# Optimization experiments

Hardware: AMD Instinct MI355X
Metric: run time of the kernel (lower is better)

Reference implementation:

```python
import jax, jax.numpy as jnp
import numpy as np

KSIZE = 3
STRIDE = 1
PADDING = 1
DILATION = 1
C_IN = 16
C_OUT = 16


def setup_inputs() -> dict:
    key = jax.random.key(0)
    k1, k2, k3 = jax.random.split(key, 3)
    inputs = jax.random.normal(k1, (2, C_IN, 24, 24, 24, 24), dtype=jnp.float32)
    weight = jax.random.normal(k2, (C_OUT, C_IN * KSIZE ** 4), dtype=jnp.float32)
    bias = jax.random.normal(k3, (1, C_OUT, 1, 1, 1, 1), dtype=jnp.float32)
    return {"inputs": inputs, "weight": weight, "bias": bias}


def reference(inputs, weight, bias):
    # weight stored flattened: [C_out, C_in * k^4] -> [C_out, C_in, k, k, k, k]
    w = weight.reshape(C_OUT, C_IN, KSIZE, KSIZE, KSIZE, KSIZE)
    # General 4-spatial-dim convolution via XLA's ND conv.
    dn = jax.lax.ConvDimensionNumbers(
        lhs_spec=(0, 1, 2, 3, 4, 5),   # N, C, U, V, H, W
        rhs_spec=(0, 1, 2, 3, 4, 5),   # O, I, kU, kV, kH, kW
        out_spec=(0, 1, 2, 3, 4, 5),
    )
    out = jax.lax.conv_general_dilated(
        inputs, w,
        window_strides=(STRIDE,) * 4,
        padding=((PADDING, PADDING),) * 4,
        rhs_dilation=(DILATION,) * 4,
        dimension_numbers=dn,
    )
    return out + bias
```

## Files before the change

kernel.cpp:

```cpp
#include <hip/hip_runtime.h>

#define S 24
#define PLANE 576
#define CISTRIDE 331776
#define SLAB_B 21632
#define QSLAB_B 6656
#define QOFF 4992
#define A_BYTES 46080
#define WS_SLABS A_BYTES

typedef __attribute__((ext_vector_type(8))) short bf16x8;
typedef __attribute__((ext_vector_type(4))) float f32x4;

__device__ __forceinline__ ushort f2bf(float f) {
    unsigned int u = __builtin_bit_cast(unsigned int, f);
    unsigned int r = u + 0x7fffu + ((u >> 16) & 1u);
    return (ushort)(r >> 16);
}

__device__ __forceinline__ int swz(int row, int col, int half) {
    return (((row * 26 + col) * 32) + half * 16) ^ ((row & 3) << 4);
}

__global__ void __launch_bounds__(256)
pack_in(const float* __restrict__ in, const float* __restrict__ wgt, char* __restrict__ ws) {
    __shared__ unsigned lds_t[16][288];

    const int b = blockIdx.x;
    const int nb = b / PLANE, uv = b % PLANE;
    const float* src = in + (size_t)nb * 16 * CISTRIDE + (size_t)uv * PLANE;
    char* dst = ws + WS_SLABS + (size_t)b * SLAB_B;
    const int t = threadIdx.x;

    float4 f[9];
    #pragma unroll
    for (int i = 0; i < 9; ++i) {
        int flat = i * 256 + t;
        int ci = flat / 144, q4 = flat % 144;
        f[i] = *(const float4*)(src + (size_t)ci * CISTRIDE + 4 * q4);
    }
    #pragma unroll
    for (int i = 0; i < 9; ++i) {
        int flat = i * 256 + t;
        int ci = flat / 144, q4 = flat % 144;
        uint2 pk;
        pk.x = (unsigned)f2bf(f[i].x) | ((unsigned)f2bf(f[i].y) << 16);
        pk.y = (unsigned)f2bf(f[i].z) | ((unsigned)f2bf(f[i].w) << 16);
        *(uint2*)&lds_t[ci][2 * q4] = pk;
    }
    __syncthreads();

    #pragma unroll
    for (int i = 0; i < 6; ++i) {
        int c = i * 256 + t;
        if (c < 1352) {
            int k = c >> 2;
            int row = k / 13;
            int pos2 = c ^ (row & 3);
            int pos = pos2 >> 1, h = pos2 & 1;
            int col = pos - row * 26;
            uint4 o = make_uint4(0, 0, 0, 0);
            if (row >= 1 && row <= 24 && col >= 1 && col <= 24) {
                int q = (row - 1) * 24 + (col - 1);
                int q2 = q >> 1, odd = q & 1;
                #pragma unroll
                for (int kk = 0; kk < 4; ++kk) {
                    unsigned a = lds_t[8 * h + 2 * kk][q2];
                    unsigned bb = lds_t[8 * h + 2 * kk + 1][q2];
                    unsigned val = odd ? ((a >> 16) | (bb & 0xffff0000u))
                                       : ((a & 0xffffu) | (bb << 16));
                    ((unsigned*)&o)[kk] = val;
                }
            }
            *(uint4*)(dst + (size_t)c * 16) = o;
        }
    }

    if (b == 0) {
        for (int i = t; i < 2880; i += 256) {
            int step = i >> 6;
            int tap = step / 5, s = step % 5;
            int lane = i & 63;
            int co = lane & 15, gA = lane >> 4;
            int o = 2 * s + (gA >> 1);
            int cib = (gA & 1) * 8;
            ushort vals[8];
            #pragma unroll
            for (int j = 0; j < 8; ++j)
                vals[j] = (o <= 8) ? f2bf(wgt[co * 1296 + (cib + j) * 81 + tap * 9 + o]) : (ushort)0;
            uint4 pk;
            pk.x = vals[0] | ((unsigned)vals[1] << 16);
            pk.y = vals[2] | ((unsigned)vals[3] << 16);
            pk.z = vals[4] | ((unsigned)vals[5] << 16);
            pk.w = vals[6] | ((unsigned)vals[7] << 16);
            *(uint4*)(ws + (size_t)i * 16) = pk;
        }
    }
}

__global__ void __launch_bounds__(192, 4)
conv4d_main(const char* __restrict__ ws, const float* __restrict__ bias,
            float* __restrict__ out) {
    __shared__ __align__(16) char lds[2 * QSLAB_B];

    const int t = threadIdx.x, lane = t & 63, wvid = t >> 6;
    const int braw = blockIdx.x;
    const int b = (braw & 7) * 288 + (braw >> 3);
    const int nb = b / 1152, rem = b % 1152;
    const int u = rem / 48, rem2 = rem % 48;
    const int v0 = (rem2 >> 2) * 2, qq = rem2 & 3;

    const int n16 = lane & 15, g = lane >> 4;
    const int dh = n16 >> 3, dw = n16 & 7;
    const int half = g & 1, osel = g >> 1;

    int laneoff[2][5];
    #pragma unroll
    for (int trp = 0; trp < 2; ++trp)
        #pragma unroll
        for (int s = 0; s < 5; ++s) {
            int o = 2 * s + osel; if (o > 8) o = 8;
            int kh = o / 3, kw = o % 3;
            int r_off = dh + kh, c_off = dw + kw;
            int lin = (r_off * 26 + c_off) * 32 + half * 16;
            laneoff[trp][s] = lin ^ ((((trp << 1) + r_off) & 3) << 4);
        }

    f32x4 acc0[3], acc1[3];
    #pragma unroll
    for (int i = 0; i < 3; ++i) { acc0[i] = (f32x4){0,0,0,0}; acc1[i] = (f32x4){0,0,0,0}; }

    unsigned mask = 0;
    #pragma unroll
    for (int i = 0; i < 12; ++i) {
        int uu = u + (i >> 2) - 1, vv = v0 + (i & 3) - 1;
        if (uu >= 0 && uu < S && vv >= 0 && vv < S) mask |= 1u << i;
    }

    const char* slabs = ws + WS_SLABS;
    const int srcoff = qq * QOFF;
    #define SLAB_PTR(i_) (slabs + ((size_t)nb * PLANE + (u + ((i_) >> 2) - 1) * S + (v0 + ((i_) & 3) - 1)) * SLAB_B + srcoff)

    #define STAGE(bufsel_, src_) do {                                              \
        const char* _s = (src_);                                                   \
        _Pragma("unroll")                                                          \
        for (int r2 = 0; r2 < 3; ++r2) {                                           \
            int chunk = r2 * 192 + t;                                              \
            if (r2 < 2 || t < 32)                                                  \
                __builtin_amdgcn_global_load_lds(                                  \
                    (const __attribute__((address_space(1))) unsigned int*)(_s + (size_t)chunk * 16), \
                    (__attribute__((address_space(3))) unsigned int*)(lds + (bufsel_) * QSLAB_B + chunk * 16), \
                    16, 0, 0);                                                     \
        }                                                                          \
    } while (0)

    const bf16x8 zfr = {0,0,0,0,0,0,0,0};

    int cur = __ffs(mask) - 1;
    int bufsel = 0;
    STAGE(0, SLAB_PTR(cur));
    __syncthreads();

    while (1) {
        unsigned remm = mask >> (cur + 1);
        int nxt = remm ? (cur + 1 + __ffs(remm) - 1) : -1;

        const int ku = cur >> 2, dv = (cur & 3) - 1;
        const bool v0ok = dv <= 1, v1ok = dv >= 0;
        const int t0i = min(ku * 3 + dv + 1, 8);
        const int t1i = max(ku * 3 + dv, 0);
        const char* ap0 = ws + (size_t)t0i * 5120 + (size_t)lane * 16;
        const char* ap1 = ws + (size_t)t1i * 5120 + (size_t)lane * 16;
        bf16x8 afr0[5], afr1[5];
        #pragma unroll
        for (int s = 0; s < 5; ++s) {
            bf16x8 r0 = *(const bf16x8*)(ap0 + s * 1024);
            bf16x8 r1 = *(const bf16x8*)(ap1 + s * 1024);
            afr0[s] = v0ok ? r0 : zfr;
            afr1[s] = v1ok ? r1 : zfr;
        }
        __builtin_amdgcn_sched_barrier(0);

        if (nxt >= 0) STAGE(bufsel ^ 1, SLAB_PTR(nxt));

        const char* bp = lds + bufsel * QSLAB_B + wvid * 256;
        #pragma unroll
        for (int tr = 0; tr < 3; ++tr) {
            const int trp = (tr + qq) & 1;
            const char* bpt = bp + tr * 1664;
            #pragma unroll
            for (int s = 0; s < 5; ++s) {
                bf16x8 bfr = *(const bf16x8*)(bpt + laneoff[trp][s]);
                acc0[tr] = __builtin_amdgcn_mfma_f32_16x16x32_bf16(afr0[s], bfr, acc0[tr], 0, 0, 0);
                acc1[tr] = __builtin_amdgcn_mfma_f32_16x16x32_bf16(afr1[s], bfr, acc1[tr], 0, 0, 0);
            }
        }
        __syncthreads();
        if (nxt < 0) break;
        cur = nxt; bufsel ^= 1;
    }

    float bv[4];
    #pragma unroll
    for (int r = 0; r < 4; ++r) bv[r] = bias[g * 4 + r];
    float* outp0 = out + (size_t)nb * 16 * CISTRIDE + (size_t)(u * S + v0) * PLANE;
    float* outp1 = outp0 + PLANE;
    #pragma unroll
    for (int tr = 0; tr < 3; ++tr) {
        int row = qq * 6 + tr * 2 + dh;
        int col = wvid * 8 + dw;
        int pos = row * S + col;
        #pragma unroll
        for (int r = 0; r < 4; ++r) {
            outp0[(size_t)(g * 4 + r) * CISTRIDE + pos] = acc0[tr][r] + bv[r];
            outp1[(size_t)(g * 4 + r) * CISTRIDE + pos] = acc1[tr][r] + bv[r];
        }
    }
}

extern "C" void kernel_launch(void* const* d_in, const int* in_sizes, int n_in,
                              void* d_out, int out_size, void* d_ws, size_t ws_size,
                              hipStream_t stream) {
    const float* in   = (const float*)d_in[0];
    const float* wgt  = (const float*)d_in[1];
    const float* bias = (const float*)d_in[2];
    float* out        = (float*)d_out;
    char* ws          = (char*)d_ws;

    pack_in<<<dim3(1152), dim3(256), 0, stream>>>(in, wgt, ws);
    conv4d_main<<<dim3(2304), dim3(192), 0, stream>>>(ws, bias, out);
}
```

Before: 82.87 us.

## Deepen conv slab pipeline to two-ahead prefetch and use a zero weight slab

The main loop now prefetches the LDS input slab two taps ahead into the buffer just consumed. It loads the next tap's weight fragments before a single barrier per iteration, using an explicit vmcnt wait in place of a full __syncthreads. Out-of-range taps point at an extra all-zero weight slab written by the pack kernel, which removes the per-fragment selects. The aim is to hide global-load latency behind the MFMA work and cut synchronisation. In exchange it relies on hand-counted vmcnt values being correct and holds more registers live.

```diff
diff --git a/kernel.cpp b/kernel.cpp
--- a/kernel.cpp
+++ b/kernel.cpp
@@ -6,7 +6,7 @@
 #define SLAB_B 21632
 #define QSLAB_B 6656
 #define QOFF 4992
-#define A_BYTES 46080
+#define A_BYTES 51200
 #define WS_SLABS A_BYTES
 
 typedef __attribute__((ext_vector_type(8))) short bf16x8;
@@ -16,10 +16,6 @@
     unsigned int u = __builtin_bit_cast(unsigned int, f);
     unsigned int r = u + 0x7fffu + ((u >> 16) & 1u);
     return (ushort)(r >> 16);
-}
-
-__device__ __forceinline__ int swz(int row, int col, int half) {
-    return (((row * 26 + col) * 32) + half * 16) ^ ((row & 3) << 4);
 }
 
 __global__ void __launch_bounds__(256)
@@ -77,7 +73,7 @@
     }
 
     if (b == 0) {
-        for (int i = t; i < 2880; i += 256) {
+        for (int i = t; i < 3200; i += 256) {
             int step = i >> 6;
             int tap = step / 5, s = step % 5;
             int lane = i & 63;
@@ -86,8 +82,11 @@
             int cib = (gA & 1) * 8;
             ushort vals[8];
             #pragma unroll
-            for (int j = 0; j < 8; ++j)
-                vals[j] = (o <= 8) ? f2bf(wgt[co * 1296 + (cib + j) * 81 + tap * 9 + o]) : (ushort)0;
+            for (int j = 0; j < 8; ++j) {
+                int widx = co * 1296 + (cib + j) * 81 + tap * 9 + o;
+                widx = widx < 20736 ? widx : 0;
+                vals[j] = (tap <= 8 && o <= 8) ? f2bf(wgt[widx]) : (ushort)0;
+            }
             uint4 pk;
             pk.x = vals[0] | ((unsigned)vals[1] << 16);
             pk.y = vals[2] | ((unsigned)vals[3] << 16);
@@ -154,36 +153,33 @@
         }                                                                          \
     } while (0)
 
-    const bf16x8 zfr = {0,0,0,0,0,0,0,0};
+    bf16x8 a0[5], a1[5];
+    #define LOAD_A(tap_) do {                                                      \
+        int _ku = (tap_) >> 2, _dv = ((tap_) & 3) - 1;                             \
+        int _s0 = (_dv <= 1) ? (_ku * 3 + _dv + 1) : 9;                            \
+        int _s1 = (_dv >= 0) ? (_ku * 3 + _dv) : 9;                                \
+        const char* _ap0 = ws + (size_t)_s0 * 5120 + (size_t)lane * 16;            \
+        const char* _ap1 = ws + (size_t)_s1 * 5120 + (size_t)lane * 16;            \
+        _Pragma("unroll")                                                          \
+        for (int s = 0; s < 5; ++s) {                                              \
+            a0[s] = *(const bf16x8*)(_ap0 + s * 1024);                             \
+            a1[s] = *(const bf16x8*)(_ap1 + s * 1024);                             \
+        }                                                                          \
+    } while (0)
 
     int cur = __ffs(mask) - 1;
-    int bufsel = 0;
+    unsigned remm = mask >> (cur + 1);
+    int nxt = remm ? (cur + 1 + __ffs(remm) - 1) : -1;
+
     STAGE(0, SLAB_PTR(cur));
-    __syncthreads();
-
+    LOAD_A(cur);
+    if (nxt >= 0) STAGE(1, SLAB_PTR(nxt));
+    asm volatile("s_waitcnt vmcnt(10)" ::: "memory");
+    __builtin_amdgcn_s_barrier();
+
+    int cb = 0;
     while (1) {
-        unsigned remm = mask >> (cur + 1);
-        int nxt = remm ? (cur + 1 + __ffs(remm) - 1) : -1;
-
-        const int ku = cur >> 2, dv = (cur & 3) - 1;
-        const bool v0ok = dv <= 1, v1ok = dv >= 0;
-        const int t0i = min(ku * 3 + dv + 1, 8);
-        const int t1i = max(ku * 3 + dv, 0);
-        const char* ap0 = ws + (size_t)t0i * 5120 + (size_t)lane * 16;
-        const char* ap1 = ws + (size_t)t1i * 5120 + (size_t)lane * 16;
-        bf16x8 afr0[5], afr1[5];
-        #pragma unroll
-        for (int s = 0; s < 5; ++s) {
-            bf16x8 r0 = *(const bf16x8*)(ap0 + s * 1024);
-            bf16x8 r1 = *(const bf16x8*)(ap1 + s * 1024);
-            afr0[s] = v0ok ? r0 : zfr;
-            afr1[s] = v1ok ? r1 : zfr;
-        }
-        __builtin_amdgcn_sched_barrier(0);
-
-        if (nxt >= 0) STAGE(bufsel ^ 1, SLAB_PTR(nxt));
-
-        const char* bp = lds + bufsel * QSLAB_B + wvid * 256;
+        const char* bp = lds + cb * QSLAB_B + wvid * 256;
         #pragma unroll
         for (int tr = 0; tr < 3; ++tr) {
             const int trp = (tr + qq) & 1;
@@ -191,13 +187,18 @@
             #pragma unroll
             for (int s = 0; s < 5; ++s) {
                 bf16x8 bfr = *(const bf16x8*)(bpt + laneoff[trp][s]);
-                acc0[tr] = __builtin_amdgcn_mfma_f32_16x16x32_bf16(afr0[s], bfr, acc0[tr], 0, 0, 0);
-                acc1[tr] = __builtin_amdgcn_mfma_f32_16x16x32_bf16(afr1[s], bfr, acc1[tr], 0, 0, 0);
+                acc0[tr] = __builtin_amdgcn_mfma_f32_16x16x32_bf16(a0[s], bfr, acc0[tr], 0, 0, 0);
+                acc1[tr] = __builtin_amdgcn_mfma_f32_16x16x32_bf16(a1[s], bfr, acc1[tr], 0, 0, 0);
             }
         }
-        __syncthreads();
         if (nxt < 0) break;
-        cur = nxt; bufsel ^= 1;
+        unsigned r2m = mask >> (nxt + 1);
+        int nxt2 = r2m ? (nxt + 1 + __ffs(r2m) - 1) : -1;
+        LOAD_A(nxt);
+        asm volatile("s_waitcnt vmcnt(10)" ::: "memory");
+        __builtin_amdgcn_s_barrier();
+        if (nxt2 >= 0) STAGE(cb, SLAB_PTR(nxt2));
+        cur = nxt; nxt = nxt2; cb ^= 1;
     }
 
     float bv[4];
```

Result: faster. 80.78 us (-2.5%).

## Compute four output v-planes per block to reuse staged input slabs

Applied to the files above, without the earlier changes.

The main conv kernel now has each block produce four adjacent v output planes instead of two. It walks 18 input slabs per ku, holds all three kv weight fragments in registers, and accumulates into 12 tiles, halving the grid and cutting redundant slab staging per output. The pack kernel now loads fp32 straight into LDS with global_load_lds and converts to bf16 when writing the swizzled output. The trade-off is higher register pressure, reflected in the occupancy hint dropping from 4 to 3, and fewer blocks in flight.

```diff
diff --git a/kernel.cpp b/kernel.cpp
--- a/kernel.cpp
+++ b/kernel.cpp
@@ -18,13 +18,9 @@
     return (ushort)(r >> 16);
 }
 
-__device__ __forceinline__ int swz(int row, int col, int half) {
-    return (((row * 26 + col) * 32) + half * 16) ^ ((row & 3) << 4);
-}
-
 __global__ void __launch_bounds__(256)
 pack_in(const float* __restrict__ in, const float* __restrict__ wgt, char* __restrict__ ws) {
-    __shared__ unsigned lds_t[16][288];
+    __shared__ __align__(16) float lds_f[16 * 576];
 
     const int b = blockIdx.x;
     const int nb = b / PLANE, uv = b % PLANE;
@@ -32,21 +28,14 @@
     char* dst = ws + WS_SLABS + (size_t)b * SLAB_B;
     const int t = threadIdx.x;
 
-    float4 f[9];
-    #pragma unroll
-    for (int i = 0; i < 9; ++i) {
-        int flat = i * 256 + t;
-        int ci = flat / 144, q4 = flat % 144;
-        f[i] = *(const float4*)(src + (size_t)ci * CISTRIDE + 4 * q4);
-    }
-    #pragma unroll
-    for (int i = 0; i < 9; ++i) {
-        int flat = i * 256 + t;
-        int ci = flat / 144, q4 = flat % 144;
-        uint2 pk;
-        pk.x = (unsigned)f2bf(f[i].x) | ((unsigned)f2bf(f[i].y) << 16);
-        pk.y = (unsigned)f2bf(f[i].z) | ((unsigned)f2bf(f[i].w) << 16);
-        *(uint2*)&lds_t[ci][2 * q4] = pk;
+    #pragma unroll
+    for (int r = 0; r < 9; ++r) {
+        int chunk = r * 256 + t;
+        int ci = chunk / 144, q4 = chunk % 144;
+        __builtin_amdgcn_global_load_lds(
+            (const __attribute__((address_space(1))) unsigned int*)(src + (size_t)ci * CISTRIDE + 4 * q4),
+            (__attribute__((address_space(3))) unsigned int*)(&lds_f[chunk * 4]),
+            16, 0, 0);
     }
     __syncthreads();
 
@@ -54,25 +43,19 @@
     for (int i = 0; i < 6; ++i) {
         int c = i * 256 + t;
         if (c < 1352) {
-            int k = c >> 2;
-            int row = k / 13;
-            int pos2 = c ^ (row & 3);
-            int pos = pos2 >> 1, h = pos2 & 1;
-            int col = pos - row * 26;
+            int pos = c >> 1, h = c & 1;
+            int row = pos / 26, col = pos % 26;
             uint4 o = make_uint4(0, 0, 0, 0);
             if (row >= 1 && row <= 24 && col >= 1 && col <= 24) {
                 int q = (row - 1) * 24 + (col - 1);
-                int q2 = q >> 1, odd = q & 1;
                 #pragma unroll
                 for (int kk = 0; kk < 4; ++kk) {
-                    unsigned a = lds_t[8 * h + 2 * kk][q2];
-                    unsigned bb = lds_t[8 * h + 2 * kk + 1][q2];
-                    unsigned val = odd ? ((a >> 16) | (bb & 0xffff0000u))
-                                       : ((a & 0xffffu) | (bb << 16));
-                    ((unsigned*)&o)[kk] = val;
+                    float fa = lds_f[(8 * h + 2 * kk) * 576 + q];
+                    float fb = lds_f[(8 * h + 2 * kk + 1) * 576 + q];
+                    ((unsigned*)&o)[kk] = (unsigned)f2bf(fa) | ((unsigned)f2bf(fb) << 16);
                 }
             }
-            *(uint4*)(dst + (size_t)c * 16) = o;
+            *(uint4*)(dst + (((size_t)c * 16) ^ (size_t)((row & 3) << 4))) = o;
         }
     }
 
@@ -98,48 +81,50 @@
     }
 }
 
-__global__ void __launch_bounds__(192, 4)
+__global__ void __launch_bounds__(192, 3)
 conv4d_main(const char* __restrict__ ws, const float* __restrict__ bias,
             float* __restrict__ out) {
     __shared__ __align__(16) char lds[2 * QSLAB_B];
 
     const int t = threadIdx.x, lane = t & 63, wvid = t >> 6;
     const int braw = blockIdx.x;
-    const int b = (braw & 7) * 288 + (braw >> 3);
-    const int nb = b / 1152, rem = b % 1152;
-    const int u = rem / 48, rem2 = rem % 48;
-    const int v0 = (rem2 >> 2) * 2, qq = rem2 & 3;
+    const int b = (braw & 7) * 144 + (braw >> 3);
+    const int nb = b / 576, rem = b % 576;
+    const int u = rem / 24, rem2 = rem % 24;
+    const int v0 = (rem2 >> 2) * 4, qq = rem2 & 3;
 
     const int n16 = lane & 15, g = lane >> 4;
     const int dh = n16 >> 3, dw = n16 & 7;
     const int half = g & 1, osel = g >> 1;
 
-    int laneoff[2][5];
-    #pragma unroll
-    for (int trp = 0; trp < 2; ++trp)
+    int loff[3][5];
+    #pragma unroll
+    for (int tr = 0; tr < 3; ++tr)
         #pragma unroll
         for (int s = 0; s < 5; ++s) {
             int o = 2 * s + osel; if (o > 8) o = 8;
             int kh = o / 3, kw = o % 3;
             int r_off = dh + kh, c_off = dw + kw;
             int lin = (r_off * 26 + c_off) * 32 + half * 16;
-            laneoff[trp][s] = lin ^ ((((trp << 1) + r_off) & 3) << 4);
-        }
-
-    f32x4 acc0[3], acc1[3];
-    #pragma unroll
-    for (int i = 0; i < 3; ++i) { acc0[i] = (f32x4){0,0,0,0}; acc1[i] = (f32x4){0,0,0,0}; }
+            loff[tr][s] = lin ^ (((qq * 6 + tr * 2 + r_off) & 3) << 4);
+        }
+
+    f32x4 acc[4][3];
+    #pragma unroll
+    for (int a = 0; a < 4; ++a)
+        #pragma unroll
+        for (int tr = 0; tr < 3; ++tr) acc[a][tr] = (f32x4){0, 0, 0, 0};
 
     unsigned mask = 0;
     #pragma unroll
-    for (int i = 0; i < 12; ++i) {
-        int uu = u + (i >> 2) - 1, vv = v0 + (i & 3) - 1;
+    for (int i = 0; i < 18; ++i) {
+        int uu = u + i / 6 - 1, vv = v0 + i % 6 - 1;
         if (uu >= 0 && uu < S && vv >= 0 && vv < S) mask |= 1u << i;
     }
 
     const char* slabs = ws + WS_SLABS;
-    const int srcoff = qq * QOFF;
-    #define SLAB_PTR(i_) (slabs + ((size_t)nb * PLANE + (u + ((i_) >> 2) - 1) * S + (v0 + ((i_) & 3) - 1)) * SLAB_B + srcoff)
+    const size_t qoff = (size_t)qq * QOFF;
+    #define SLAB_PTR(i_) (slabs + ((size_t)nb * PLANE + (u + (i_) / 6 - 1) * S + (v0 + (i_) % 6 - 1)) * SLAB_B + qoff)
 
     #define STAGE(bufsel_, src_) do {                                              \
         const char* _s = (src_);                                                   \
@@ -154,66 +139,63 @@
         }                                                                          \
     } while (0)
 
-    const bf16x8 zfr = {0,0,0,0,0,0,0,0};
-
-    int cur = __ffs(mask) - 1;
-    int bufsel = 0;
-    STAGE(0, SLAB_PTR(cur));
+    int first = __ffs(mask) - 1;
+    STAGE(0, SLAB_PTR(first));
     __syncthreads();
 
-    while (1) {
-        unsigned remm = mask >> (cur + 1);
-        int nxt = remm ? (cur + 1 + __ffs(remm) - 1) : -1;
-
-        const int ku = cur >> 2, dv = (cur & 3) - 1;
-        const bool v0ok = dv <= 1, v1ok = dv >= 0;
-        const int t0i = min(ku * 3 + dv + 1, 8);
-        const int t1i = max(ku * 3 + dv, 0);
-        const char* ap0 = ws + (size_t)t0i * 5120 + (size_t)lane * 16;
-        const char* ap1 = ws + (size_t)t1i * 5120 + (size_t)lane * 16;
-        bf16x8 afr0[5], afr1[5];
-        #pragma unroll
-        for (int s = 0; s < 5; ++s) {
-            bf16x8 r0 = *(const bf16x8*)(ap0 + s * 1024);
-            bf16x8 r1 = *(const bf16x8*)(ap1 + s * 1024);
-            afr0[s] = v0ok ? r0 : zfr;
-            afr1[s] = v1ok ? r1 : zfr;
-        }
-        __builtin_amdgcn_sched_barrier(0);
-
-        if (nxt >= 0) STAGE(bufsel ^ 1, SLAB_PTR(nxt));
-
-        const char* bp = lds + bufsel * QSLAB_B + wvid * 256;
+    int cb = 0;
+    bf16x8 afr[3][5];
+
+    #pragma unroll
+    for (int ku = 0; ku < 3; ++ku) {
+        if (!((mask >> (ku * 6)) & 63u)) continue;
+        #pragma unroll
+        for (int kv = 0; kv < 3; ++kv) {
+            const char* ap = ws + (size_t)(ku * 3 + kv) * 5120 + (size_t)lane * 16;
+            #pragma unroll
+            for (int s = 0; s < 5; ++s) afr[kv][s] = *(const bf16x8*)(ap + s * 1024);
+        }
+        #pragma unroll
+        for (int vj = 0; vj < 6; ++vj) {
+            const int i = ku * 6 + vj;
+            if (!(mask & (1u << i))) continue;
+            unsigned rm = mask >> (i + 1);
+            int nx = rm ? (i + 1 + __ffs(rm) - 1) : -1;
+            if (nx >= 0) STAGE(cb ^ 1, SLAB_PTR(nx));
+
+            const char* bp = lds + cb * QSLAB_B + wvid * 256;
+            #pragma unroll
+            for (int tr = 0; tr < 3; ++tr) {
+                #pragma unroll
+                for (int s = 0; s < 5; ++s) {
+                    bf16x8 bfr = *(const bf16x8*)(bp + tr * 1664 + loff[tr][s]);
+                    #pragma unroll
+                    for (int kv = 0; kv < 3; ++kv) {
+                        const int a = vj - kv;
+                        if (a >= 0 && a <= 3)
+                            acc[a][tr] = __builtin_amdgcn_mfma_f32_16x16x32_bf16(afr[kv][s], bfr, acc[a][tr], 0, 0, 0);
+                    }
+                }
+            }
+            __syncthreads();
+            cb ^= 1;
+        }
+    }
+
+    float bv[4];
+    #pragma unroll
+    for (int r = 0; r < 4; ++r) bv[r] = bias[g * 4 + r];
+    #pragma unroll
+    for (int a = 0; a < 4; ++a) {
+        float* outp = out + (size_t)nb * 16 * CISTRIDE + (size_t)(u * S + v0 + a) * PLANE;
         #pragma unroll
         for (int tr = 0; tr < 3; ++tr) {
-            const int trp = (tr + qq) & 1;
-            const char* bpt = bp + tr * 1664;
-            #pragma unroll
-            for (int s = 0; s < 5; ++s) {
-                bf16x8 bfr = *(const bf16x8*)(bpt + laneoff[trp][s]);
-                acc0[tr] = __builtin_amdgcn_mfma_f32_16x16x32_bf16(afr0[s], bfr, acc0[tr], 0, 0, 0);
-                acc1[tr] = __builtin_amdgcn_mfma_f32_16x16x32_bf16(afr1[s], bfr, acc1[tr], 0, 0, 0);
-            }
-        }
-        __syncthreads();
-        if (nxt < 0) break;
-        cur = nxt; bufsel ^= 1;
-    }
-
-    float bv[4];
-    #pragma unroll
-    for (int r = 0; r < 4; ++r) bv[r] = bias[g * 4 + r];
-    float* outp0 = out + (size_t)nb * 16 * CISTRIDE + (size_t)(u * S + v0) * PLANE;
-    float* outp1 = outp0 + PLANE;
-    #pragma unroll
-    for (int tr = 0; tr < 3; ++tr) {
-        int row = qq * 6 + tr * 2 + dh;
-        int col = wvid * 8 + dw;
-        int pos = row * S + col;
-        #pragma unroll
-        for (int r = 0; r < 4; ++r) {
-            outp0[(size_t)(g * 4 + r) * CISTRIDE + pos] = acc0[tr][r] + bv[r];
-            outp1[(size_t)(g * 4 + r) * CISTRIDE + pos] = acc1[tr][r] + bv[r];
+            int row = qq * 6 + tr * 2 + dh;
+            int col = wvid * 8 + dw;
+            int pos = row * S + col;
+            #pragma unroll
+            for (int r = 0; r < 4; ++r)
+                outp[(size_t)(g * 4 + r) * CISTRIDE + pos] = acc[a][tr][r] + bv[r];
         }
     }
 }
@@ -228,5 +210,5 @@
     char* ws          = (char*)d_ws;
 
     pack_in<<<dim3(1152), dim3(256), 0, stream>>>(in, wgt, ws);
-    conv4d_main<<<dim3(2304), dim3(192), 0, stream>>>(ws, bias, out);
-}
+    conv4d_main<<<dim3(1152), dim3(192), 0, stream>>>(ws, bias, out);
+}
```

New measurement: 72.74 us. 1.14x faster.
